# Kernel optimization log

Hardware: AMD Instinct MI355X
Metric: run time of the kernel (lower is better)

The kernel has to match this reference:

```python
import jax, jax.numpy as jnp
import numpy as np

B, S, D = 2, 2048, 1024
H, DK = 16, 64          # n_heads, d_kv; inner_dim = H*DK = D
NUM_BUCKETS = 32        # T5 relative_attention_num_buckets
MAX_DIST = 128          # T5 relative_attention_max_distance
SM_SCALE = 1.0 / np.sqrt(H)  # module uses 1/sqrt(n_heads), not 1/sqrt(d_kv)


def setup_inputs() -> dict:
    key = jax.random.key(0)
    ks = jax.random.split(key, 6)
    w = 0.02  # typical init scale for projection weights
    return {
        "hidden_states": jax.random.normal(ks[0], (B, S, D), jnp.float32),
        "Wq": jax.random.normal(ks[1], (D, H * DK), jnp.float32) * w,
        "Wk": jax.random.normal(ks[2], (D, H * DK), jnp.float32) * w,
        "Wv": jax.random.normal(ks[3], (D, H * DK), jnp.float32) * w,
        "Wo": jax.random.normal(ks[4], (H * DK, D), jnp.float32) * w,
        "rel_bias": jax.random.normal(ks[5], (NUM_BUCKETS, H), jnp.float32) * w,
    }


def _relative_position_buckets(qlen, klen):
    """T5 bidirectional relative-position bucketing -> [qlen, klen] int32."""
    ctx = jnp.arange(qlen, dtype=jnp.int32)[:, None]
    mem = jnp.arange(klen, dtype=jnp.int32)[None, :]
    rp = mem - ctx  # relative position
    nb = NUM_BUCKETS // 2  # bidirectional split
    ret = (rp > 0).astype(jnp.int32) * nb
    rpa = jnp.abs(rp)
    max_exact = nb // 2
    is_small = rpa < max_exact
    rpf = jnp.maximum(rpa, 1).astype(jnp.float32)
    large = max_exact + (
        jnp.log(rpf / max_exact) / np.log(MAX_DIST / max_exact) * (nb - max_exact)
    ).astype(jnp.int32)
    large = jnp.minimum(large, nb - 1)
    return ret + jnp.where(is_small, rpa, large)


def reference(hidden_states, Wq, Wk, Wv, Wo, rel_bias):
    b, s, d = hidden_states.shape
    q = (hidden_states @ Wq).reshape(b, s, H, DK)
    k = (hidden_states @ Wk).reshape(b, s, H, DK)
    v = (hidden_states @ Wv).reshape(b, s, H, DK)

    buckets = _relative_position_buckets(s, s)        # [S, S]
    bias = rel_bias[buckets]                          # [S, S, H]
    bias = jnp.transpose(bias, (2, 0, 1))[None]       # [1, H, S, S]

    scores = jnp.einsum("bqhd,bkhd->bhqk", q, k) * SM_SCALE + bias
    attn = jax.nn.softmax(scores, axis=-1)
    out = jnp.einsum("bhqk,bkhd->bqhd", attn, v).reshape(b, s, H * DK)
    return out @ Wo
```

## Files before the change

### kernel.cpp

```cpp
#include <hip/hip_runtime.h>
#include <math.h>


typedef _Float16 f16;
typedef _Float16 f16x4 __attribute__((ext_vector_type(4)));
typedef _Float16 f16x8 __attribute__((ext_vector_type(8)));
typedef float f32x4 __attribute__((ext_vector_type(4)));
typedef float f32x16 __attribute__((ext_vector_type(16)));
typedef unsigned int u32;
typedef u32 u32x4 __attribute__((ext_vector_type(4)));

#define MFMA16(a, b, c) __builtin_amdgcn_mfma_f32_16x16x32_f16((a), (b), (c), 0, 0, 0)
#define MFMA32(a, b, c) __builtin_amdgcn_mfma_f32_32x32x16_f16((a), (b), (c), 0, 0, 0)

static __device__ __forceinline__ float EXP2(float x) {
  float r;
  asm("v_exp_f32 %0, %1" : "=v"(r) : "v"(x));
  return r;
}

static __device__ __forceinline__ u32 pk2(float a, float b) {
  return __builtin_bit_cast(u32, __builtin_amdgcn_cvt_pkrtz(a, b));
}
static __device__ __forceinline__ void swap32(u32& a, u32& b) {
  asm volatile("v_permlane32_swap_b32 %0, %1" : "+v"(a), "+v"(b));
}

#define KEEPV8(v8)                                                        \
  do {                                                                    \
    u32x4 _t = __builtin_bit_cast(u32x4, (v8));                           \
    asm volatile("" ::"v"(_t[0]), "v"(_t[1]), "v"(_t[2]), "v"(_t[3]));    \
  } while (0)

__device__ __forceinline__ void gload16(const f16* g, f16* l) {
  __builtin_amdgcn_global_load_lds(
      (const __attribute__((address_space(1))) void*)g,
      (__attribute__((address_space(3))) void*)l, 16, 0, 0);
}

__global__ void prep_kernel(const float* __restrict__ X, const float* __restrict__ w0,
                            const float* __restrict__ w1, const float* __restrict__ w2,
                            const float* __restrict__ w3, const float* __restrict__ relb,
                            f16x4* __restrict__ xh, f16* __restrict__ wt,
                            f16* __restrict__ bias_rel) {
  const int z = blockIdx.z;
  const int tx = threadIdx.x, ty = threadIdx.y;
  if (z < 4) {
    const float* w = (z == 0) ? w0 : (z == 1) ? w1 : (z == 2) ? w2 : w3;
    float sc = (z == 0) ? 0.36067376022224085f : 1.0f;
    __shared__ float tile[32][33];
    int kt = blockIdx.x * 32, nt = blockIdx.y * 32;
#pragma unroll
    for (int i = 0; i < 4; ++i)
      tile[ty + i * 8][tx] = w[(size_t)(kt + ty + i * 8) * 1024 + nt + tx];
    __syncthreads();
#pragma unroll
    for (int i = 0; i < 4; ++i)
      wt[((size_t)z * 1024 + nt + ty + i * 8) * 1024 + kt + tx] =
          (f16)(tile[tx][ty + i * 8] * sc);
  } else if (z == 4) {
    if (blockIdx.x >= 8) return;
    int idx = (blockIdx.x * 32 + blockIdx.y) * 256 + ty * 32 + tx;
    int h = idx >> 12;
    int r = idx & 4095;
    int rp = r - 2048;
    if (rp < -2047) rp = -2047;
    int bucket = (rp > 0) ? 16 : 0;
    int rpa = (rp < 0) ? -rp : rp;
    if (rpa < 8) {
      bucket += rpa;
    } else {
      int large = 8 + (int)(logf((float)rpa / 8.0f) / logf(16.0f) * 8.0f);
      bucket += (large < 15) ? large : 15;
    }
    bias_rel[idx] = (f16)(relb[bucket * 16 + h] * 1.4426950408889634f);
  } else {
    const float4* x4 = (const float4*)X;
    int i = (blockIdx.x * 32 + blockIdx.y) * 256 + ty * 32 + tx;
#pragma unroll
    for (int rep = 0; rep < 4; ++rep, i += 262144) {
      float4 v = x4[i];
      f16x4 o;
      o[0] = (f16)v.x; o[1] = (f16)v.y; o[2] = (f16)v.z; o[3] = (f16)v.w;
      xh[i] = o;
    }
  }
}

__device__ __forceinline__ void gemm128_core(const f16* __restrict__ A, const f16* __restrict__ Bt,
                                             int mrow, int ncol0, f16* sm ,
                                             f32x4 acc[4][4]) {
  const int t = threadIdx.x;
  const int lane = t & 63, w = t >> 6;
  const int cL = lane & 15, g = lane >> 4;
  const int wr = w >> 1, wc = w & 1;

  const int c0 = w * 128 + lane;
  const int c1 = c0 + 64;
  const int rA0 = c0 >> 2, kA0 = ((c0 & 3) ^ (rA0 & 3)) << 3;
  const int rA1 = c1 >> 2, kA1 = ((c1 & 3) ^ (rA1 & 3)) << 3;
  const f16* gA0 = A + (size_t)(mrow + rA0) * 1024 + kA0;
  const f16* gA1 = A + (size_t)(mrow + rA1) * 1024 + kA1;
  const f16* gB0 = Bt + (size_t)(ncol0 + rA0) * 1024 + kA0;
  const f16* gB1 = Bt + (size_t)(ncol0 + rA1) * 1024 + kA1;
  const int lds0 = (w * 2) * 512, lds1 = (w * 2 + 1) * 512;

#define GSTAGE(buf, k0)                            \
  do {                                             \
    f16* s_ = sm + (buf) * 8192;                   \
    gload16(gA0 + (k0), s_ + lds0);                \
    gload16(gA1 + (k0), s_ + lds1);                \
    gload16(gB0 + (k0), s_ + 4096 + lds0);         \
    gload16(gB1 + (k0), s_ + 4096 + lds1);         \
  } while (0)

  GSTAGE(0, 0);
  __syncthreads();
#pragma unroll 2
  for (int ks = 0; ks < 32; ++ks) {
    const int cur = ks & 1;
    if (ks < 31) GSTAGE(cur ^ 1, (ks + 1) * 32);
    const f16* bA = sm + cur * 8192;
    const f16* bB = bA + 4096;
    f16x8 af[4], bf[4];
#pragma unroll
    for (int m = 0; m < 4; ++m) {
      int r = wr * 64 + m * 16 + cL;
      af[m] = *(const f16x8*)&bA[r * 32 + ((g ^ (r & 3)) << 3)];
    }
#pragma unroll
    for (int n = 0; n < 4; ++n) {
      int r = wc * 64 + n * 16 + cL;
      bf[n] = *(const f16x8*)&bB[r * 32 + ((g ^ (r & 3)) << 3)];
    }
#pragma unroll
    for (int m = 0; m < 4; ++m)
#pragma unroll
      for (int n = 0; n < 4; ++n) acc[m][n] = MFMA16(af[m], bf[n], acc[m][n]);
    __syncthreads();
  }
#undef GSTAGE
}

__global__ __launch_bounds__(256) void gemm_qkv_kernel(const f16* __restrict__ Xh,
                                                       const f16* __restrict__ Wt,
                                                       f16* __restrict__ Qh,
                                                       f16* __restrict__ Kh,
                                                       f16* __restrict__ Vt) {
  __shared__ __align__(16) f16 sm[2][8192];
  int mrow = blockIdx.y * 128, ncol0 = blockIdx.x * 128;
  f32x4 acc[4][4] = {};
  gemm128_core(Xh, Wt, mrow, ncol0, &sm[0][0], acc);
  int lane = threadIdx.x & 63, w = threadIdx.x >> 6;
  int cL = lane & 15, g = lane >> 4;
  int wr = w >> 1, wc = w & 1;
  int which = (ncol0 + wc * 64) >> 10;
#pragma unroll
  for (int m = 0; m < 4; ++m) {
#pragma unroll
    for (int n = 0; n < 4; ++n) {
#pragma unroll
      for (int r = 0; r < 4; ++r) {
        int tt = mrow + wr * 64 + m * 16 + g * 4 + r;
        int b = tt >> 11, s = tt & 2047;
        int col = (ncol0 + wc * 64 + n * 16 + cL) & 1023;
        int hh = col >> 6, dk = col & 63;
        f16 val = (f16)acc[m][n][r];
        if (which == 0)
          Qh[(((size_t)b * 16 + hh) * 2048 + s) * 64 + dk] = val;
        else if (which == 1)
          Kh[(((size_t)b * 16 + hh) * 2048 + s) * 64 + dk] = val;
        else
          Vt[(((size_t)b * 16 + hh) * 64 + dk) * 2048 + s] = val;
      }
    }
  }
}

__global__ __launch_bounds__(256) void gemm_out_kernel(const f16* __restrict__ Oh,
                                                       const f16* __restrict__ WoT,
                                                       float* __restrict__ out) {
  __shared__ __align__(16) f16 sm[2][8192];
  int mrow = blockIdx.y * 128, ncol0 = blockIdx.x * 128;
  f32x4 acc[4][4] = {};
  gemm128_core(Oh, WoT, mrow, ncol0, &sm[0][0], acc);
  int lane = threadIdx.x & 63, w = threadIdx.x >> 6;
  int cL = lane & 15, g = lane >> 4;
  int wr = w >> 1, wc = w & 1;
#pragma unroll
  for (int m = 0; m < 4; ++m)
#pragma unroll
    for (int n = 0; n < 4; ++n)
#pragma unroll
      for (int r = 0; r < 4; ++r) {
        int tt = mrow + wr * 64 + m * 16 + g * 4 + r;
        out[(size_t)tt * 1024 + ncol0 + wc * 64 + n * 16 + cL] = acc[m][n][r];
      }
}

__global__ __launch_bounds__(512) void attn_kernel(const f16* __restrict__ Qh,
                                                   const f16* __restrict__ Kh,
                                                   const f16* __restrict__ Vt,
                                                   const f16* __restrict__ bias_rel,
                                                   f16* __restrict__ Oh) {
  __shared__ __align__(16) f16 sKV[2][4][8192];
  __shared__ __align__(16) f16 sB[2176];
  const int p = blockIdx.x;
  const int L = ((p & 7) << 6) + (p >> 3);
  const int bh = L >> 4;
  const int qt = (L & 15) << 7;
  const int h = bh & 15, b = bh >> 4;
  int t = threadIdx.x;
  int lane = t & 63, wave = t >> 6;
  const int gr = wave >> 2, sw = wave & 3;
  int lo5 = lane & 31, hi = lane >> 5;
  const size_t bhS = (size_t)bh * 2048;
  const int qrow = qt + sw * 32 + lo5;

  const f16* qp = Qh + (bhS + qrow) * 64 + hi * 8;
  f16x8 qf[4];
#pragma unroll
  for (int m = 0; m < 4; ++m) qf[m] = *(const f16x8*)(qp + 16 * m);

  float cpos = (float)bias_rel[(size_t)h * 4096 + 4095];
  float cneg = (float)bias_rel[(size_t)h * 4096 + 1];

#pragma unroll
  for (int m = 0; m < 4; ++m) KEEPV8(qf[m]);
  asm volatile("" ::"v"(cpos), "v"(cneg));

  {
    const float4* gB = (const float4*)(bias_rel + (size_t)h * 4096 + 1920 - qt);
    for (int i = t; i < 272; i += 512) ((float4*)sB)[i] = gB[i];
  }

  const int tg = t & 255;
  const int rK0 = tg >> 3, ccK0 = ((tg & 7) ^ (rK0 & 7)) << 3;
  const int rK1 = rK0 + 32, ccK1 = ((tg & 7) ^ (rK1 & 7)) << 3;
  const f16* gK0 = Kh + (bhS + rK0) * 64 + ccK0;
  const f16* gK1 = Kh + (bhS + rK1) * 64 + ccK1;
  const f16* gV0 = Vt + ((size_t)bh * 64 + rK0) * 2048 + ccK0;
  const f16* gV1 = Vt + ((size_t)bh * 64 + rK1) * 2048 + ccK1;
  const int ldsA = sw * 512, ldsB = sw * 512 + 2048;

#define ASTAGE(buf, key0)                           \
  do {                                              \
    f16* s_ = &sKV[gr][buf][0];                     \
    gload16(gK0 + (size_t)(key0) * 64, s_ + ldsA);  \
    gload16(gK1 + (size_t)(key0) * 64, s_ + ldsB);  \
    gload16(gV0 + (key0), s_ + 4096 + ldsA);        \
    gload16(gV1 + (key0), s_ + 4096 + ldsB);        \
  } while (0)

  f32x16 o0 = {}, o1 = {};
  float m_ = -INFINITY, lsum = 0.f;
  const int sw7 = lo5 & 7;
  const int kbase = gr << 10;

  auto qk = [&](const f16* kb, f32x16& s0, f32x16& s1) {
    const f16* kr0 = kb + lo5 * 64;
    const f16* kr1 = kb + (32 + lo5) * 64;
#pragma unroll
    for (int m = 0; m < 4; ++m) {
      int c = ((2 * m + hi) ^ sw7) << 3;
      s0 = MFMA32(*(const f16x8*)(kr0 + c), qf[m], s0);
      s1 = MFMA32(*(const f16x8*)(kr1 + c), qf[m], s1);
    }
  };
  auto rowmax = [&](const f32x16& a, const f32x16& bvec) -> float {
    float tm[16];
#pragma unroll
    for (int i = 0; i < 16; ++i) tm[i] = fmaxf(a[i], bvec[i]);
#pragma unroll
    for (int s2 = 8; s2; s2 >>= 1)
#pragma unroll
      for (int i = 0; i < 8; ++i)
        if (i < s2) tm[i] = fmaxf(tm[i], tm[i + s2]);
    return tm[0];
  };
  auto softpack = [&](const f32x16& s0, const f32x16& s1, f16x8& b0, f16x8& b1, f16x8& b2,
                      f16x8& b3) -> float {
    float pr[16];
    u32 w0, w1, w2, w3, w4, w5, w6, w7;
#pragma unroll
    for (int i = 0; i < 16; ++i) pr[i] = EXP2(s0[i] - m_);
    w0 = pk2(pr[0], pr[1]);   w1 = pk2(pr[2], pr[3]);
    w2 = pk2(pr[4], pr[5]);   w3 = pk2(pr[6], pr[7]);
    w4 = pk2(pr[8], pr[9]);   w5 = pk2(pr[10], pr[11]);
    w6 = pk2(pr[12], pr[13]); w7 = pk2(pr[14], pr[15]);
#pragma unroll
    for (int s2 = 8; s2; s2 >>= 1)
#pragma unroll
      for (int i = 0; i < 8; ++i)
        if (i < s2) pr[i] += pr[i + s2];
    float ls = pr[0];
    swap32(w0, w2); swap32(w1, w3); swap32(w4, w6); swap32(w5, w7);
    b0 = __builtin_bit_cast(f16x8, (u32x4){w0, w1, w2, w3});
    b1 = __builtin_bit_cast(f16x8, (u32x4){w4, w5, w6, w7});
#pragma unroll
    for (int i = 0; i < 16; ++i) pr[i] = EXP2(s1[i] - m_);
    w0 = pk2(pr[0], pr[1]);   w1 = pk2(pr[2], pr[3]);
    w2 = pk2(pr[4], pr[5]);   w3 = pk2(pr[6], pr[7]);
    w4 = pk2(pr[8], pr[9]);   w5 = pk2(pr[10], pr[11]);
    w6 = pk2(pr[12], pr[13]); w7 = pk2(pr[14], pr[15]);
#pragma unroll
    for (int s2 = 8; s2; s2 >>= 1)
#pragma unroll
      for (int i = 0; i < 8; ++i)
        if (i < s2) pr[i] += pr[i + s2];
    ls += pr[0];
    swap32(w0, w2); swap32(w1, w3); swap32(w4, w6); swap32(w5, w7);
    b2 = __builtin_bit_cast(f16x8, (u32x4){w0, w1, w2, w3});
    b3 = __builtin_bit_cast(f16x8, (u32x4){w4, w5, w6, w7});
    return ls;
  };
  auto pv = [&](const f16* vb, const f16x8& b0, const f16x8& b1, const f16x8& b2,
                const f16x8& b3) {
    const f16* vr0 = vb + lo5 * 64;
    const f16* vr1 = vb + (32 + lo5) * 64;
    {
      int c = ((0 + hi) ^ sw7) << 3;
      o0 = MFMA32(*(const f16x8*)(vr0 + c), b0, o0);
      o1 = MFMA32(*(const f16x8*)(vr1 + c), b0, o1);
    }
    {
      int c = ((2 + hi) ^ sw7) << 3;
      o0 = MFMA32(*(const f16x8*)(vr0 + c), b1, o0);
      o1 = MFMA32(*(const f16x8*)(vr1 + c), b1, o1);
    }
    {
      int c = ((4 + hi) ^ sw7) << 3;
      o0 = MFMA32(*(const f16x8*)(vr0 + c), b2, o0);
      o1 = MFMA32(*(const f16x8*)(vr1 + c), b2, o1);
    }
    {
      int c = ((6 + hi) ^ sw7) << 3;
      o0 = MFMA32(*(const f16x8*)(vr0 + c), b3, o0);
      o1 = MFMA32(*(const f16x8*)(vr1 + c), b3, o1);
    }
  };
  auto biasinit = [&](int key0, f32x16& s0, f32x16& s1) {
    const int dkt = key0 - qt;
    if (dkt >= 256 || dkt <= -192) {
      float c = (dkt > 0) ? cpos : cneg;
#pragma unroll
      for (int i = 0; i < 16; ++i) { s0[i] = c; s1[i] = c; }
    } else {
      const int bb = key0 + 4 * hi - sw * 32 - lo5 + 128;
#pragma unroll
      for (int i = 0; i < 16; ++i) {
        int pat = (i & 3) + 8 * (i >> 2);
        s0[i] = (float)sB[bb + pat];
        s1[i] = (float)sB[bb + 32 + pat];
      }
    }
  };

  ASTAGE(0, kbase);
  ASTAGE(1, kbase + 64);
  asm volatile("s_waitcnt lgkmcnt(0)" ::: "memory");

  for (int pp = 0; pp < 8; ++pp) {
    asm volatile("s_waitcnt vmcnt(0)" ::: "memory");
    __builtin_amdgcn_s_barrier();
    if (pp < 7) {
      ASTAGE((2 * pp + 2) & 3, kbase + (2 * pp + 2) * 64);
      ASTAGE((2 * pp + 3) & 3, kbase + (2 * pp + 3) * 64);
    }
    const int keyA = kbase + 2 * pp * 64;
    const f16* bufA = &sKV[gr][(2 * pp) & 3][0];
    const f16* bufB = &sKV[gr][(2 * pp + 1) & 3][0];

    f32x16 saA0, saA1, saB0, saB1;
    biasinit(keyA, saA0, saA1);
    biasinit(keyA + 64, saB0, saB1);
    __builtin_amdgcn_s_setprio(1);
    qk(bufA, saA0, saA1);
    qk(bufB, saB0, saB1);
    __builtin_amdgcn_s_setprio(0);

    float mx = fmaxf(rowmax(saA0, saA1), rowmax(saB0, saB1));
    mx = fmaxf(mx, __shfl_xor(mx, 32));
    if (__any(mx > m_ + 8.f)) {
      float mn = fmaxf(m_, mx);
      float corr = EXP2(m_ - mn);
      lsum *= corr;
      m_ = mn;
#pragma unroll
      for (int i = 0; i < 16; ++i) { o0[i] *= corr; o1[i] *= corr; }
    }

    f16x8 f0, f1, f2, f3;
    lsum += softpack(saA0, saA1, f0, f1, f2, f3);
    __builtin_amdgcn_s_setprio(1);
    pv(bufA + 4096, f0, f1, f2, f3);
    __builtin_amdgcn_s_setprio(0);
    lsum += softpack(saB0, saB1, f0, f1, f2, f3);
    __builtin_amdgcn_s_setprio(1);
    pv(bufB + 4096, f0, f1, f2, f3);
    __builtin_amdgcn_s_setprio(0);
  }
#undef ASTAGE

  __syncthreads();
  float* sX = (float*)&sKV[0][0][0];
  const int slot = (sw * 64 + lane) * 35;
  if (gr == 1) {
#pragma unroll
    for (int i = 0; i < 16; ++i) {
      sX[slot + i] = o0[i];
      sX[slot + 16 + i] = o1[i];
    }
    sX[slot + 32] = m_;
    sX[slot + 33] = lsum;
  }
  __syncthreads();
  if (gr == 0) {
    float m2 = sX[slot + 32], l2 = sX[slot + 33];
    float mn = fmaxf(m_, m2);
    float c1 = EXP2(m_ - mn), c2 = EXP2(m2 - mn);
    float s = lsum * c1 + l2 * c2;
    s += __shfl_xor(s, 32);
    float inv = 1.0f / s;
    size_t base = ((size_t)b * 2048 + qrow) * 1024 + h * 64 + 4 * hi;
#pragma unroll
    for (int rq = 0; rq < 4; ++rq) {
      f16x4 v0, v1;
#pragma unroll
      for (int j = 0; j < 4; ++j) {
        v0[j] = (f16)((o0[rq * 4 + j] * c1 + sX[slot + rq * 4 + j] * c2) * inv);
        v1[j] = (f16)((o1[rq * 4 + j] * c1 + sX[slot + 16 + rq * 4 + j] * c2) * inv);
      }
      *(f16x4*)&Oh[base + 8 * rq] = v0;
      *(f16x4*)&Oh[base + 32 + 8 * rq] = v1;
    }
  }
}


extern "C" void kernel_launch(void* const* d_in, const int* in_sizes, int n_in,
                              void* d_out, int out_size, void* d_ws, size_t ws_size,
                              hipStream_t stream) {
  const float* X = (const float*)d_in[0];
  const float* Wq = (const float*)d_in[1];
  const float* Wk = (const float*)d_in[2];
  const float* Wv = (const float*)d_in[3];
  const float* Wo = (const float*)d_in[4];
  const float* relb = (const float*)d_in[5];

  const size_t MB8 = (size_t)8 << 20;
  if (ws_size < 6 * MB8 + (1 << 19)) return;

  char* ws = (char*)d_ws;
  f16* Xh = (f16*)(ws + 0 * MB8);
  f16* Wt = (f16*)(ws + 1 * MB8);
  f16* Qh = (f16*)(ws + 2 * MB8);
  f16* Kh = (f16*)(ws + 3 * MB8);
  f16* Vt = (f16*)(ws + 4 * MB8);
  f16* Oh = (f16*)(ws + 5 * MB8);
  f16* brel = (f16*)(ws + 6 * MB8);

  prep_kernel<<<dim3(32, 32, 6), dim3(32, 8), 0, stream>>>(X, Wq, Wk, Wv, Wo, relb,
                                                           (f16x4*)Xh, Wt, brel);
  gemm_qkv_kernel<<<dim3(24, 32), dim3(256), 0, stream>>>(Xh, Wt, Qh, Kh, Vt);
  attn_kernel<<<dim3(512), dim3(512), 0, stream>>>(Qh, Kh, Vt, brel, Oh);
  gemm_out_kernel<<<dim3(8, 32), dim3(256), 0, stream>>>(Oh, Wt + (size_t)3072 * 1024,
                                                         (float*)d_out);
}
```

Baseline: 138.6 us.

## Replace QKV projection GEMM with 256x256-tile pipelined 8-wave kernel

Swaps the 128x128-tile QKV GEMM for a 256x256-tile kernel with 512 threads, a 64-wide K step and a double-buffered LDS ring. Global loads are staged in quarters, interleaved with MFMA work, and separated by explicit vmcnt waits and barriers. It also uses s_setprio around the MFMA bursts and remaps block IDs so neighbouring blocks share tiles. The larger tile raises data reuse per loaded byte but leaves only 192 blocks (fewer than the CU count), uses more registers and LDS, and reduces occupancy.

```diff
diff --git a/kernel.cpp b/kernel.cpp
--- a/kernel.cpp
+++ b/kernel.cpp
@@ -87,6 +87,132 @@
   }
 }
 
+
+#define FDECL f16x8 af[4][2]; f16x8 bf[2][2]
+#define FRAGS(S, Q)                                                                 \
+  {                                                                                 \
+    const f16* bA_ = sAf + (S) * 16384;                                             \
+    const f16* bB_ = sBf + (S) * 16384;                                             \
+    const int mb_ = wr * 128 + ((Q) >> 1) * 64;                                     \
+    const int nb_ = wc * 64 + ((Q) & 1) * 32;                                       \
+    _Pragma("unroll") for (int mf = 0; mf < 4; ++mf) {                              \
+      int r_ = mb_ + mf * 16 + cL;                                                  \
+      _Pragma("unroll") for (int ks = 0; ks < 2; ++ks)                              \
+          af[mf][ks] =                                                              \
+          *(const f16x8*)&bA_[r_ * 64 + ((((ks << 2) | g) ^ (r_ & 7)) << 3)];       \
+    }                                                                               \
+    _Pragma("unroll") for (int nf = 0; nf < 2; ++nf) {                              \
+      int r_ = nb_ + nf * 16 + cL;                                                  \
+      _Pragma("unroll") for (int ks = 0; ks < 2; ++ks)                              \
+          bf[nf][ks] =                                                              \
+          *(const f16x8*)&bB_[r_ * 64 + ((((ks << 2) | g) ^ (r_ & 7)) << 3)];       \
+    }                                                                               \
+  }
+#define MFMAQ(Q)                                                                    \
+  {                                                                                 \
+    __builtin_amdgcn_s_setprio(1);                                                  \
+    _Pragma("unroll") for (int mf = 0; mf < 4; ++mf)                                \
+        _Pragma("unroll") for (int nf = 0; nf < 2; ++nf)                            \
+            _Pragma("unroll") for (int ks = 0; ks < 2; ++ks)                        \
+                acc[((Q) >> 1) * 4 + mf][((Q) & 1) * 2 + nf] =                      \
+        MFMA16(af[mf][ks], bf[nf][ks],                                              \
+               acc[((Q) >> 1) * 4 + mf][((Q) & 1) * 2 + nf]);                       \
+    __builtin_amdgcn_s_setprio(0);                                                  \
+  }
+#define BARX __builtin_amdgcn_s_barrier()
+#define VW2 asm volatile("s_waitcnt vmcnt(2)" ::: "memory")
+#define VW0 asm volatile("s_waitcnt vmcnt(0)" ::: "memory")
+#define STG_A(S, kt, h)                                                             \
+  {                                                                                 \
+    gload16(gAp[2 * (h)] + (size_t)(kt) * 64,                                       \
+            sAf + (S) * 16384 + w * 512 + (2 * (h)) * 4096);                        \
+    gload16(gAp[2 * (h) + 1] + (size_t)(kt) * 64,                                   \
+            sAf + (S) * 16384 + w * 512 + (2 * (h) + 1) * 4096);                    \
+  }
+#define STG_B(S, kt, h)                                                             \
+  {                                                                                 \
+    gload16(gBp[2 * (h)] + (size_t)(kt) * 64,                                       \
+            sBf + (S) * 16384 + w * 512 + (2 * (h)) * 4096);                        \
+    gload16(gBp[2 * (h) + 1] + (size_t)(kt) * 64,                                   \
+            sBf + (S) * 16384 + w * 512 + (2 * (h) + 1) * 4096);                    \
+  }
+
+__global__ __launch_bounds__(512) void gemm_qkv256_kernel(const f16* __restrict__ Xh,
+                                                          const f16* __restrict__ Wt,
+                                                          f16* __restrict__ Qh,
+                                                          f16* __restrict__ Kh,
+                                                          f16* __restrict__ Vt) {
+  __shared__ __align__(16) f16 sA[2][16384];
+  __shared__ __align__(16) f16 sB[2][16384];
+  f16* sAf = &sA[0][0];
+  f16* sBf = &sB[0][0];
+  const int p = blockIdx.x;
+  const int L = (p & 7) * 24 + (p >> 3);
+  const int bx = L % 12, by = L / 12;
+  const int mrow0 = by * 256, ncol0 = bx * 256;
+  const int t = threadIdx.x, lane = t & 63, w = t >> 6;
+  const int wr = w >> 2, wc = w & 3;
+  const int cL = lane & 15, g = lane >> 4;
+
+  const int c0 = w * 64 + lane;
+  const f16* gAp[4];
+  const f16* gBp[4];
+#pragma unroll
+  for (int i = 0; i < 4; ++i) {
+    int c = c0 + 512 * i;
+    int row = c >> 3;
+    int col8 = ((c & 7) ^ (row & 7)) << 3;
+    gAp[i] = Xh + (size_t)(mrow0 + row) * 1024 + col8;
+    gBp[i] = Wt + (size_t)(ncol0 + row) * 1024 + col8;
+  }
+
+  f32x4 acc[8][4] = {};
+
+  STG_A(0, 0, 0); STG_A(0, 0, 1); STG_B(0, 0, 0); STG_B(0, 0, 1);
+
+#pragma unroll 1
+  for (int it = 0; it < 8; ++it) {
+    const int kt1 = 2 * it + 1, kt2 = 2 * it + 2;
+    { FDECL; STG_A(1, kt1, 0); VW2; BARX; FRAGS(0, 0); MFMAQ(0); BARX; }
+    { FDECL; FRAGS(0, 1); STG_A(1, kt1, 1); BARX; MFMAQ(1); BARX; }
+    { FDECL; FRAGS(0, 2); STG_B(1, kt1, 0); BARX; MFMAQ(2); BARX; }
+    { FDECL; FRAGS(0, 3); STG_B(1, kt1, 1); BARX; MFMAQ(3); BARX; }
+    if (it < 7) {
+      { FDECL; STG_A(0, kt2, 0); VW2; BARX; FRAGS(1, 0); MFMAQ(0); BARX; }
+      { FDECL; FRAGS(1, 1); STG_A(0, kt2, 1); BARX; MFMAQ(1); BARX; }
+      { FDECL; FRAGS(1, 2); STG_B(0, kt2, 0); BARX; MFMAQ(2); BARX; }
+      { FDECL; FRAGS(1, 3); STG_B(0, kt2, 1); BARX; MFMAQ(3); BARX; }
+    } else {
+      { FDECL; VW0; BARX; FRAGS(1, 0); MFMAQ(0); BARX; }
+      { FDECL; FRAGS(1, 1); BARX; MFMAQ(1); BARX; }
+      { FDECL; FRAGS(1, 2); BARX; MFMAQ(2); BARX; }
+      { FDECL; FRAGS(1, 3); BARX; MFMAQ(3); BARX; }
+    }
+  }
+
+  const int which = (ncol0 + wc * 64) >> 10;
+#pragma unroll
+  for (int mf = 0; mf < 8; ++mf) {
+#pragma unroll
+    for (int nf = 0; nf < 4; ++nf) {
+#pragma unroll
+      for (int j = 0; j < 4; ++j) {
+        int tt = mrow0 + wr * 128 + mf * 16 + g * 4 + j;
+        int b = tt >> 11, s = tt & 2047;
+        int col = (ncol0 + wc * 64 + nf * 16 + cL) & 1023;
+        int hh = col >> 6, dk = col & 63;
+        f16 val = (f16)acc[mf][nf][j];
+        if (which == 0)
+          Qh[(((size_t)b * 16 + hh) * 2048 + s) * 64 + dk] = val;
+        else if (which == 1)
+          Kh[(((size_t)b * 16 + hh) * 2048 + s) * 64 + dk] = val;
+        else
+          Vt[(((size_t)b * 16 + hh) * 64 + dk) * 2048 + s] = val;
+      }
+    }
+  }
+}
+
 __device__ __forceinline__ void gemm128_core(const f16* __restrict__ A, const f16* __restrict__ Bt,
                                              int mrow, int ncol0, f16* sm ,
                                              f32x4 acc[4][4]) {
@@ -140,41 +266,6 @@
     __syncthreads();
   }
 #undef GSTAGE
-}
-
-__global__ __launch_bounds__(256) void gemm_qkv_kernel(const f16* __restrict__ Xh,
-                                                       const f16* __restrict__ Wt,
-                                                       f16* __restrict__ Qh,
-                                                       f16* __restrict__ Kh,
-                                                       f16* __restrict__ Vt) {
-  __shared__ __align__(16) f16 sm[2][8192];
-  int mrow = blockIdx.y * 128, ncol0 = blockIdx.x * 128;
-  f32x4 acc[4][4] = {};
-  gemm128_core(Xh, Wt, mrow, ncol0, &sm[0][0], acc);
-  int lane = threadIdx.x & 63, w = threadIdx.x >> 6;
-  int cL = lane & 15, g = lane >> 4;
-  int wr = w >> 1, wc = w & 1;
-  int which = (ncol0 + wc * 64) >> 10;
-#pragma unroll
-  for (int m = 0; m < 4; ++m) {
-#pragma unroll
-    for (int n = 0; n < 4; ++n) {
-#pragma unroll
-      for (int r = 0; r < 4; ++r) {
-        int tt = mrow + wr * 64 + m * 16 + g * 4 + r;
-        int b = tt >> 11, s = tt & 2047;
-        int col = (ncol0 + wc * 64 + n * 16 + cL) & 1023;
-        int hh = col >> 6, dk = col & 63;
-        f16 val = (f16)acc[m][n][r];
-        if (which == 0)
-          Qh[(((size_t)b * 16 + hh) * 2048 + s) * 64 + dk] = val;
-        else if (which == 1)
-          Kh[(((size_t)b * 16 + hh) * 2048 + s) * 64 + dk] = val;
-        else
-          Vt[(((size_t)b * 16 + hh) * 64 + dk) * 2048 + s] = val;
-      }
-    }
-  }
 }
 
 __global__ __launch_bounds__(256) void gemm_out_kernel(const f16* __restrict__ Oh,
@@ -462,7 +553,7 @@
 
   prep_kernel<<<dim3(32, 32, 6), dim3(32, 8), 0, stream>>>(X, Wq, Wk, Wv, Wo, relb,
                                                            (f16x4*)Xh, Wt, brel);
-  gemm_qkv_kernel<<<dim3(24, 32), dim3(256), 0, stream>>>(Xh, Wt, Qh, Kh, Vt);
+  gemm_qkv256_kernel<<<dim3(192), dim3(512), 0, stream>>>(Xh, Wt, Qh, Kh, Vt);
   attn_kernel<<<dim3(512), dim3(512), 0, stream>>>(Qh, Kh, Vt, brel, Oh);
   gemm_out_kernel<<<dim3(8, 32), dim3(256), 0, stream>>>(Oh, Wt + (size_t)3072 * 1024,
                                                          (float*)d_out);
```

Result: slower. 229.2 us (+65.3%).
